# Kernel optimization log

Hardware: AMD Instinct MI355X
Metric: run time of the kernel (lower is better)

Reference implementation:

```python
import jax, jax.numpy as jnp
import numpy as np

N_HEADS = 16


def setup_inputs() -> dict:
    key = jax.random.key(0)
    ks = jax.random.split(key, 4)
    B, S, E = 4, 2048, 1024
    x = jax.random.normal(ks[0], (B, S, E), dtype=jnp.float32)
    w_attn = jax.random.normal(ks[1], (E, 3 * E), dtype=jnp.float32) * 0.02
    b_attn = jnp.zeros((3 * E,), dtype=jnp.float32)
    w_proj = jax.random.normal(ks[2], (E, E), dtype=jnp.float32) * 0.02
    b_proj = jnp.zeros((E,), dtype=jnp.float32)
    return {"x": x, "w_attn": w_attn, "b_attn": b_attn, "w_proj": w_proj, "b_proj": b_proj}


def reference(x, w_attn, b_attn, w_proj, b_proj):
    B, S, E = x.shape
    H = N_HEADS
    D = E // H
    # fused QKV projection (Conv1D: x @ W + b)
    qkv = x @ w_attn + b_attn                     # [B, S, 3E]
    q, k, v = jnp.split(qkv, 3, axis=-1)          # each [B, S, E]
    q = q.reshape(B, S, H, D).transpose(0, 2, 1, 3)  # [B, H, S, D]
    k = k.reshape(B, S, H, D).transpose(0, 2, 1, 3)
    v = v.reshape(B, S, H, D).transpose(0, 2, 1, 3)
    # scaled QK^T
    scores = jnp.einsum('bhqd,bhkd->bhqk', q, k) / jnp.sqrt(jnp.asarray(D, dtype=x.dtype))
    # causal mask via where with dtype-min fill (matches torch.where(c_m, w, finfo.min))
    causal = jnp.tril(jnp.ones((S, S), dtype=bool))  # [S, S]
    scores = jnp.where(causal[None, None, :, :], scores, jnp.finfo(scores.dtype).min)
    attn = jax.nn.softmax(scores, axis=-1)        # [B, H, S, S]
    o = jnp.einsum('bhqk,bhkd->bhqd', attn, v)    # [B, H, S, D]
    o = o.transpose(0, 2, 1, 3).reshape(B, S, E)  # merge heads
    return o @ w_proj + b_proj                    # output projection
```

## Files before the change

### kernel.cpp

```cpp
#include <hip/hip_runtime.h>
#include <stdint.h>


typedef __bf16 bf16;
typedef __bf16 bf16x4 __attribute__((ext_vector_type(4)));
typedef __bf16 bf16x8 __attribute__((ext_vector_type(8)));
typedef float  f32x4  __attribute__((ext_vector_type(4)));

#define DEV __device__ __forceinline__

DEV void async_copy16(bf16* lds, const bf16* g) {
  __builtin_amdgcn_global_load_lds(
      (__attribute__((address_space(1))) void*)(uintptr_t)g,
      (__attribute__((address_space(3))) void*)(uint32_t)(uintptr_t)lds,
      16, 0, 0);
}

__global__ __launch_bounds__(256) void cast_x_kernel(const float* __restrict__ in,
                                                     bf16* __restrict__ out, int n4) {
  int i = blockIdx.x * blockDim.x + threadIdx.x;
  int stride = gridDim.x * blockDim.x;
  for (; i < n4; i += stride) {
    float4 v = ((const float4*)in)[i];
    bf16x4 o = { (bf16)v.x, (bf16)v.y, (bf16)v.z, (bf16)v.w };
    *(bf16x4*)(out + (size_t)i * 4) = o;
  }
}

__global__ __launch_bounds__(256) void transpose_cast_kernel(const float* __restrict__ W,
                                                             bf16* __restrict__ Wt,
                                                             int Kd, int Nd) {
  __shared__ alignas(16) bf16 T[64 * 80];
  const int t = threadIdx.x;
  const int n0 = blockIdx.x * 64;
  const int k0 = blockIdx.y * 64;
#pragma unroll
  for (int i = 0; i < 4; ++i) {
    int idx = t + i * 256;
    int r  = idx >> 4;
    int c4 = (idx & 15) * 4;
    float4 v = *(const float4*)(W + (size_t)(k0 + r) * Nd + n0 + c4);
    bf16x4 o = { (bf16)v.x, (bf16)v.y, (bf16)v.z, (bf16)v.w };
    *(bf16x4*)(&T[r * 80 + c4]) = o;
  }
  __syncthreads();
#pragma unroll
  for (int i = 0; i < 2; ++i) {
    int idx = t + i * 256;
    int n = idx >> 3;
    int c = idx & 7;
    bf16x8 o;
#pragma unroll
    for (int j = 0; j < 8; ++j) o[j] = T[(c * 8 + j) * 80 + n];
    *(bf16x8*)(Wt + (size_t)(n0 + n) * Kd + k0 + c * 8) = o;
  }
}

__global__ __launch_bounds__(256) void vtrans_kernel(const bf16* __restrict__ qkv,
                                                     bf16* __restrict__ vt) {
  __shared__ alignas(16) bf16 T[64 * 80];
  const int t  = threadIdx.x;
  const int s0 = blockIdx.x * 64;
  const int bh = blockIdx.y;
  const int b = bh >> 4, h = bh & 15;
#pragma unroll
  for (int i = 0; i < 2; ++i) {
    int idx = t + i * 256;
    int s = idx >> 3, c = idx & 7;
    bf16x8 v = *(const bf16x8*)(qkv + (size_t)(b * 2048 + s0 + s) * 3072 + 2048 + h * 64 + c * 8);
    *(bf16x8*)(&T[s * 80 + c * 8]) = v;
  }
  __syncthreads();
#pragma unroll
  for (int i = 0; i < 2; ++i) {
    int idx = t + i * 256;
    int d = idx >> 3, c = idx & 7;
    bf16x8 o;
#pragma unroll
    for (int j = 0; j < 8; ++j) {
      int pos = c * 8 + j;
      int key = (pos & 32) | (((pos >> 2) & 1) << 4) | (((pos >> 3) & 3) << 2) | (pos & 3);
      o[j] = T[key * 80 + d];
    }
    *(bf16x8*)(vt + (size_t)(bh * 64 + d) * 2048 + s0 + c * 8) = o;
  }
}

template <typename OutT>
__global__ __launch_bounds__(512, 2) void gemm256_kernel(const bf16* __restrict__ A,
                                                         const bf16* __restrict__ Bt,
                                                         const float* __restrict__ bias,
                                                         OutT* __restrict__ C,
                                                         int M, int N, int K,
                                                         float qscale, int qcols,
                                                         int nbx) {
  __shared__ alignas(16) bf16 As[3][256 * 64];
  __shared__ alignas(16) bf16 Bs[3][128 * 64];

  const int tid  = threadIdx.x;
  const int lane = tid & 63;
  const int w    = tid >> 6;
  const int wm = w >> 1, wn = w & 1;
  const int l15 = lane & 15, l16 = lane >> 4;

  const int nwg = (int)gridDim.x;
  const int cpx = nwg >> 3;
  const int swz = ((int)blockIdx.x & 7) * cpx + ((int)blockIdx.x >> 3);
  const int m0 = (swz / nbx) * 256;
  const int n0 = (swz % nbx) * 128;

  const int srow = tid >> 3;
  const int sc   = tid & 7;
#define STAGE_HALF(buf, kt, H)                                                  \
  {                                                                             \
    const int k0_ = (kt) * 64;                                                  \
    _Pragma("unroll")                                                           \
    for (int j = 2 * (H); j < 2 * (H) + 2; ++j) {                               \
      int row = j * 64 + srow;                                                  \
      const bf16* src = A + (size_t)(m0 + row) * K + k0_ + 8 * (sc ^ (row & 7));\
      async_copy16(&As[buf][(j * 512 + w * 64) * 8], src);                      \
    }                                                                           \
    {                                                                           \
      int row = (H) * 64 + srow;                                                \
      const bf16* src = Bt + (size_t)(n0 + row) * K + k0_ + 8 * (sc ^ (row & 7));\
      async_copy16(&Bs[buf][((H) * 512 + w * 64) * 8], src);                    \
    }                                                                           \
  }

  f32x4 acc[4][4];
  f32x4 zf = {0.f, 0.f, 0.f, 0.f};
#pragma unroll
  for (int i = 0; i < 4; ++i)
#pragma unroll
    for (int j = 0; j < 4; ++j) acc[i][j] = zf;

  const int KT = K >> 6;
  STAGE_HALF(0, 0, 0) STAGE_HALF(0, 0, 1)
  STAGE_HALF(1, 1, 0) STAGE_HALF(1, 1, 1)

#define MFMA_HALF(buf, MLO)                                                     \
  {                                                                             \
    __builtin_amdgcn_s_setprio(1);                                              \
    _Pragma("unroll")                                                           \
    for (int m = (MLO); m < (MLO) + 2; ++m) {                                   \
      int ra = wm * 64 + m * 16 + l15;                                          \
      bf16x8 a0 = *(const bf16x8*)(&As[buf][ra * 64 + 8 * ((0 + l16) ^ (ra & 7))]); \
      bf16x8 a1 = *(const bf16x8*)(&As[buf][ra * 64 + 8 * ((4 + l16) ^ (ra & 7))]); \
      _Pragma("unroll")                                                         \
      for (int n = 0; n < 4; ++n)                                               \
        acc[m][n] = __builtin_amdgcn_mfma_f32_16x16x32_bf16(a0, bfr[n][0], acc[m][n], 0, 0, 0); \
      _Pragma("unroll")                                                         \
      for (int n = 0; n < 4; ++n)                                               \
        acc[m][n] = __builtin_amdgcn_mfma_f32_16x16x32_bf16(a1, bfr[n][1], acc[m][n], 0, 0, 0); \
    }                                                                           \
    __builtin_amdgcn_s_setprio(0);                                              \
  }

  int bufc = 0;
  int bufs = 2;
  for (int kt = 0; kt < KT - 1; ++kt) {
    asm volatile("s_waitcnt vmcnt(6)" ::: "memory");
    __builtin_amdgcn_s_barrier();
    asm volatile("" ::: "memory");
    const bool st = (kt + 2 < KT);
    if (st) STAGE_HALF(bufs, kt + 2, 0)
    bf16x8 bfr[4][2];
#pragma unroll
    for (int n = 0; n < 4; ++n) {
      int rb = wn * 64 + n * 16 + l15;
#pragma unroll
      for (int kk = 0; kk < 2; ++kk)
        bfr[n][kk] = *(const bf16x8*)(&Bs[bufc][rb * 64 + 8 * ((kk * 4 + l16) ^ (rb & 7))]);
    }
    MFMA_HALF(bufc, 0)
    asm volatile("" ::: "memory");
    __builtin_amdgcn_s_barrier();
    asm volatile("" ::: "memory");
    if (st) STAGE_HALF(bufs, kt + 2, 1)
    MFMA_HALF(bufc, 2)
    asm volatile("" ::: "memory");
    bufc = (bufc == 2) ? 0 : bufc + 1;
    bufs = (bufs == 2) ? 0 : bufs + 1;
  }
  asm volatile("s_waitcnt vmcnt(0)" ::: "memory");
  __builtin_amdgcn_s_barrier();
  asm volatile("" ::: "memory");
  {
    bf16x8 bfr[4][2];
#pragma unroll
    for (int n = 0; n < 4; ++n) {
      int rb = wn * 64 + n * 16 + l15;
#pragma unroll
      for (int kk = 0; kk < 2; ++kk)
        bfr[n][kk] = *(const bf16x8*)(&Bs[bufc][rb * 64 + 8 * ((kk * 4 + l16) ^ (rb & 7))]);
    }
    MFMA_HALF(bufc, 0)
    MFMA_HALF(bufc, 2)
  }

#pragma unroll
  for (int n = 0; n < 4; ++n) {
    int col = n0 + wn * 64 + n * 16 + l15;
    float bb = bias[col];
    float sc2 = (col < qcols) ? qscale : 1.0f;
#pragma unroll
    for (int m = 0; m < 4; ++m) {
#pragma unroll
      for (int reg = 0; reg < 4; ++reg) {
        int row = m0 + wm * 64 + m * 16 + l16 * 4 + reg;
        C[(size_t)row * N + col] = (OutT)((acc[m][n][reg] + bb) * sc2);
      }
    }
  }
#undef STAGE_HALF
#undef MFMA_HALF
}

__global__ __launch_bounds__(512, 4) void flash_kernel(const bf16* __restrict__ qkv,
                                                       const bf16* __restrict__ vt,
                                                       bf16* __restrict__ obuf) {
  constexpr int S = 2048, E3 = 3072;
  __shared__ alignas(16) bf16 Ks[2][64 * 64];
  __shared__ alignas(16) bf16 Vs[2][64 * 64];

  const int tid  = threadIdx.x;
  const int lane = tid & 63;
  const int w    = tid >> 6;
  const int bx = blockIdx.x;
  const int bh = blockIdx.y;
  const int b = bh >> 4, h = bh & 15;
  const int l15 = lane & 15, l16 = lane >> 4;

  const int sr  = w * 8 + (lane >> 3);
  const int scc = lane & 7;
  const bf16* kstage = qkv + (size_t)(b * S + sr) * E3 + 1024 + h * 64 + 8 * (scc ^ (sr & 7));
  const bf16* vstage = vt + (size_t)(bh * 64 + sr) * S + 8 * (scc ^ (sr & 7));

  const int xsw = l15 & 7;
  const uint32_t rdA = (uint32_t)(l15 * 128 + 16 * (l16 ^ xsw));
  const uint32_t rdB = (uint32_t)(l15 * 128 + 16 * ((4 + l16) ^ xsw));

#define KV_STAGE(buf, kv0_)                                        \
  {                                                                \
    async_copy16(Ks[buf] + w * 512, kstage + (size_t)(kv0_) * E3); \
    async_copy16(Vs[buf] + w * 512, vstage + (kv0_));              \
  }

  for (int half = 0; half < 2; ++half) {
    const int t = half ? (15 - bx) : bx;
    const int q0 = t * 128;
    const int wq0 = q0 + w * 16;
    const int nsteps = 2 * t + 2;

    KV_STAGE(0, 0)

    bf16x8 qf[2];
    {
      const bf16* qbase = qkv + (size_t)(b * S + wq0 + l15) * E3 + h * 64;
#pragma unroll
      for (int dk = 0; dk < 2; ++dk)
        qf[dk] = *(const bf16x8*)(qbase + (dk * 4 + l16) * 8);
    }

    float lstate = 0.f;
    f32x4 oacc[4];
    f32x4 zf = {0.f, 0.f, 0.f, 0.f};
#pragma unroll
    for (int i = 0; i < 4; ++i) oacc[i] = zf;

    __syncthreads();

#define FLASH_STEP(CUR, STEPIDX)                                                  \
    {                                                                             \
      const int kv0 = (STEPIDX) * 64;                                             \
      if ((STEPIDX) + 1 < nsteps) KV_STAGE((CUR) ^ 1, kv0 + 64)                   \
      if (kv0 <= wq0 + 15) {                     \
        f32x4 sv[4];                                                              \
        _Pragma("unroll")                                                         \
        for (int kf = 0; kf < 4; ++kf) sv[kf] = zf;                               \
        __builtin_amdgcn_s_setprio(1);                                            \
        _Pragma("unroll")                                                         \
        for (int kf = 0; kf < 4; ++kf) {                                          \
          bf16x8 k0 = *(const bf16x8*)((const char*)Ks[CUR] + rdA + kf * 2048);   \
          sv[kf] = __builtin_amdgcn_mfma_f32_16x16x32_bf16(k0, qf[0], sv[kf], 0, 0, 0); \
          bf16x8 k1 = *(const bf16x8*)((const char*)Ks[CUR] + rdB + kf * 2048);   \
          sv[kf] = __builtin_amdgcn_mfma_f32_16x16x32_bf16(k1, qf[1], sv[kf], 0, 0, 0); \
        }                                                                         \
        __builtin_amdgcn_s_setprio(0);                                            \
        if (kv0 + 63 > wq0) {     \
          const int qrow_ = wq0 + l15;                                            \
          _Pragma("unroll")                                                       \
          for (int kf = 0; kf < 4; ++kf)                                          \
            _Pragma("unroll")                                                     \
            for (int reg = 0; reg < 4; ++reg) {                                   \
              int key = kv0 + kf * 16 + l16 * 4 + reg;                            \
              if (key > qrow_) sv[kf][reg] = -1e30f;                              \
            }                                                                     \
        }                                                                         \
        float rsum = 0.f;                                                         \
        _Pragma("unroll")                                                         \
        for (int kf = 0; kf < 4; ++kf)                                            \
          _Pragma("unroll")                                                       \
          for (int reg = 0; reg < 4; ++reg) {                                     \
            float p = __builtin_amdgcn_exp2f(sv[kf][reg]);                        \
            sv[kf][reg] = p;                                                      \
            rsum += p;                                                            \
          }                                                                       \
        rsum += __shfl_xor(rsum, 16);                                             \
        rsum += __shfl_xor(rsum, 32);                                             \
        lstate += rsum;                                                           \
             \
        bf16x8 pb[2];                                                             \
        _Pragma("unroll")                                                         \
        for (int kc = 0; kc < 2; ++kc) {                                          \
          bf16x8 tq;                                                              \
          tq[0] = (bf16)sv[2 * kc][0];  tq[1] = (bf16)sv[2 * kc][1];              \
          tq[2] = (bf16)sv[2 * kc][2];  tq[3] = (bf16)sv[2 * kc][3];              \
          tq[4] = (bf16)sv[2 * kc + 1][0]; tq[5] = (bf16)sv[2 * kc + 1][1];       \
          tq[6] = (bf16)sv[2 * kc + 1][2]; tq[7] = (bf16)sv[2 * kc + 1][3];       \
          pb[kc] = tq;                                                            \
        }                                                                         \
        __builtin_amdgcn_s_setprio(1);                                            \
        _Pragma("unroll")                                                         \
        for (int nf = 0; nf < 4; ++nf) {                                          \
          bf16x8 vf0 = *(const bf16x8*)((const char*)Vs[CUR] + rdA + nf * 2048);  \
          oacc[nf] = __builtin_amdgcn_mfma_f32_16x16x32_bf16(vf0, pb[0], oacc[nf], 0, 0, 0); \
          bf16x8 vf1 = *(const bf16x8*)((const char*)Vs[CUR] + rdB + nf * 2048);  \
          oacc[nf] = __builtin_amdgcn_mfma_f32_16x16x32_bf16(vf1, pb[1], oacc[nf], 0, 0, 0); \
        }                                                                         \
        __builtin_amdgcn_s_setprio(0);                                            \
      }                                                                           \
      __syncthreads();          \
    }

    for (int step = 0; step < nsteps; step += 2) {
      FLASH_STEP(0, step)
      FLASH_STEP(1, step + 1)
    }
#undef FLASH_STEP

    float inv = 1.0f / lstate;
    int qrow = wq0 + l15;
#pragma unroll
    for (int nf = 0; nf < 4; ++nf) {
      bf16x4 o4 = { (bf16)(oacc[nf][0] * inv), (bf16)(oacc[nf][1] * inv),
                    (bf16)(oacc[nf][2] * inv), (bf16)(oacc[nf][3] * inv) };
      *(bf16x4*)(obuf + (size_t)(b * S + qrow) * 1024 + h * 64 + nf * 16 + l16 * 4) = o4;
    }
  }
#undef KV_STAGE
}

extern "C" void kernel_launch(void* const* d_in, const int* in_sizes, int n_in,
                              void* d_out, int out_size, void* d_ws, size_t ws_size,
                              hipStream_t stream) {
  (void)in_sizes; (void)n_in; (void)out_size; (void)ws_size;
  const float* x      = (const float*)d_in[0];
  const float* w_attn = (const float*)d_in[1];
  const float* b_attn = (const float*)d_in[2];
  const float* w_proj = (const float*)d_in[3];
  const float* b_proj = (const float*)d_in[4];
  float* out = (float*)d_out;

  char* ws = (char*)d_ws;
  bf16* xb  = (bf16*)(ws + 0);
  bf16* wat = (bf16*)(ws + 16777216);
  bf16* wpt = (bf16*)(ws + 23068672);
  bf16* qkv = (bf16*)(ws + 25165824);
  bf16* vt  = (bf16*)(ws + 75497472);
  bf16* ob  = (bf16*)(ws + 92274688);

  const float QSCALE = 0.18033688011112042f;

  cast_x_kernel<<<2048, 256, 0, stream>>>(x, xb, 8192 * 1024 / 4);
  transpose_cast_kernel<<<dim3(48, 16), 256, 0, stream>>>(w_attn, wat, 1024, 3072);
  transpose_cast_kernel<<<dim3(16, 16), 256, 0, stream>>>(w_proj, wpt, 1024, 1024);
  gemm256_kernel<bf16><<<768, 512, 0, stream>>>(xb, wat, b_attn, qkv,
                                                8192, 3072, 1024, QSCALE, 1024, 24);
  vtrans_kernel<<<dim3(32, 64), 256, 0, stream>>>(qkv, vt);
  flash_kernel<<<dim3(8, 64), 512, 0, stream>>>(qkv, vt, ob);
  gemm256_kernel<float><<<256, 512, 0, stream>>>(ob, wpt, b_proj, out,
                                                 8192, 1024, 1024, 1.0f, 0, 8);
}
```

Baseline: 163.6 us.

## Halve GEMM K-tile for higher occupancy and split flash blocks per query tile

The GEMM kernel's K-tile drops from 64 to 32, so LDS per block halves and launch bounds rise to 4 blocks per CU. The staging, swizzle and MFMA loop are restructured into one barrier per K step, with the tail folded into the main loop. The flash kernel no longer pairs a short and a long causal tile in one block. It launches one block per query tile, in reverse order, with higher launch bounds. This trades per-block load balancing and K-step amortization for more concurrent blocks, at some risk of register pressure and more barriers.

```diff
diff --git a/kernel.cpp b/kernel.cpp
--- a/kernel.cpp
+++ b/kernel.cpp
@@ -87,15 +87,15 @@
 }
 
 template <typename OutT>
-__global__ __launch_bounds__(512, 2) void gemm256_kernel(const bf16* __restrict__ A,
+__global__ __launch_bounds__(512, 4) void gemm256_kernel(const bf16* __restrict__ A,
                                                          const bf16* __restrict__ Bt,
                                                          const float* __restrict__ bias,
                                                          OutT* __restrict__ C,
                                                          int M, int N, int K,
                                                          float qscale, int qcols,
                                                          int nbx) {
-  __shared__ alignas(16) bf16 As[3][256 * 64];
-  __shared__ alignas(16) bf16 Bs[3][128 * 64];
+  __shared__ alignas(16) bf16 As[3][256 * 32];
+  __shared__ alignas(16) bf16 Bs[3][128 * 32];
 
   const int tid  = threadIdx.x;
   const int lane = tid & 63;
@@ -109,22 +109,19 @@
   const int m0 = (swz / nbx) * 256;
   const int n0 = (swz % nbx) * 128;
 
-  const int srow = tid >> 3;
-  const int sc   = tid & 7;
-#define STAGE_HALF(buf, kt, H)                                                  \
-  {                                                                             \
-    const int k0_ = (kt) * 64;                                                  \
-    _Pragma("unroll")                                                           \
-    for (int j = 2 * (H); j < 2 * (H) + 2; ++j) {                               \
-      int row = j * 64 + srow;                                                  \
-      const bf16* src = A + (size_t)(m0 + row) * K + k0_ + 8 * (sc ^ (row & 7));\
-      async_copy16(&As[buf][(j * 512 + w * 64) * 8], src);                      \
-    }                                                                           \
-    {                                                                           \
-      int row = (H) * 64 + srow;                                                \
-      const bf16* src = Bt + (size_t)(n0 + row) * K + k0_ + 8 * (sc ^ (row & 7));\
-      async_copy16(&Bs[buf][((H) * 512 + w * 64) * 8], src);                    \
-    }                                                                           \
+  const int c0  = w * 64 + lane;
+  const int rA0 = c0 >> 2, sA0 = c0 & 3;
+  const int rA1 = rA0 + 128;
+  const bf16* srcA0 = A  + (size_t)(m0 + rA0) * K + 8 * (sA0 ^ ((rA0 >> 1) & 3));
+  const bf16* srcA1 = A  + (size_t)(m0 + rA1) * K + 8 * (sA0 ^ ((rA1 >> 1) & 3));
+  const bf16* srcB  = Bt + (size_t)(n0 + rA0) * K + 8 * (sA0 ^ ((rA0 >> 1) & 3));
+
+#define STAGE_TILE(buf, kt)                                       \
+  {                                                               \
+    const int k0_ = (kt) * 32;                                    \
+    async_copy16(&As[buf][(w * 64) * 8],         srcA0 + k0_);    \
+    async_copy16(&As[buf][(512 + w * 64) * 8],   srcA1 + k0_);    \
+    async_copy16(&Bs[buf][(w * 64) * 8],         srcB  + k0_);    \
   }
 
   f32x4 acc[4][4];
@@ -134,68 +131,42 @@
 #pragma unroll
     for (int j = 0; j < 4; ++j) acc[i][j] = zf;
 
-  const int KT = K >> 6;
-  STAGE_HALF(0, 0, 0) STAGE_HALF(0, 0, 1)
-  STAGE_HALF(1, 1, 0) STAGE_HALF(1, 1, 1)
-
-#define MFMA_HALF(buf, MLO)                                                     \
-  {                                                                             \
-    __builtin_amdgcn_s_setprio(1);                                              \
-    _Pragma("unroll")                                                           \
-    for (int m = (MLO); m < (MLO) + 2; ++m) {                                   \
-      int ra = wm * 64 + m * 16 + l15;                                          \
-      bf16x8 a0 = *(const bf16x8*)(&As[buf][ra * 64 + 8 * ((0 + l16) ^ (ra & 7))]); \
-      bf16x8 a1 = *(const bf16x8*)(&As[buf][ra * 64 + 8 * ((4 + l16) ^ (ra & 7))]); \
-      _Pragma("unroll")                                                         \
-      for (int n = 0; n < 4; ++n)                                               \
-        acc[m][n] = __builtin_amdgcn_mfma_f32_16x16x32_bf16(a0, bfr[n][0], acc[m][n], 0, 0, 0); \
-      _Pragma("unroll")                                                         \
-      for (int n = 0; n < 4; ++n)                                               \
-        acc[m][n] = __builtin_amdgcn_mfma_f32_16x16x32_bf16(a1, bfr[n][1], acc[m][n], 0, 0, 0); \
-    }                                                                           \
-    __builtin_amdgcn_s_setprio(0);                                              \
-  }
+  const int KT = K >> 5;
+  STAGE_TILE(0, 0)
+  STAGE_TILE(1, 1)
+
+  const int soff = 8 * (l16 ^ ((l15 >> 1) & 3));
 
   int bufc = 0;
   int bufs = 2;
-  for (int kt = 0; kt < KT - 1; ++kt) {
-    asm volatile("s_waitcnt vmcnt(6)" ::: "memory");
+  for (int kt = 0; kt < KT; ++kt) {
+    if (kt < KT - 1) { asm volatile("s_waitcnt vmcnt(3)" ::: "memory"); }
+    else             { asm volatile("s_waitcnt vmcnt(0)" ::: "memory"); }
     __builtin_amdgcn_s_barrier();
     asm volatile("" ::: "memory");
-    const bool st = (kt + 2 < KT);
-    if (st) STAGE_HALF(bufs, kt + 2, 0)
-    bf16x8 bfr[4][2];
+    if (kt + 2 < KT) STAGE_TILE(bufs, kt + 2)
+
+    bf16x8 bfr[4], afr[4];
 #pragma unroll
     for (int n = 0; n < 4; ++n) {
       int rb = wn * 64 + n * 16 + l15;
-#pragma unroll
-      for (int kk = 0; kk < 2; ++kk)
-        bfr[n][kk] = *(const bf16x8*)(&Bs[bufc][rb * 64 + 8 * ((kk * 4 + l16) ^ (rb & 7))]);
-    }
-    MFMA_HALF(bufc, 0)
-    asm volatile("" ::: "memory");
-    __builtin_amdgcn_s_barrier();
-    asm volatile("" ::: "memory");
-    if (st) STAGE_HALF(bufs, kt + 2, 1)
-    MFMA_HALF(bufc, 2)
+      bfr[n] = *(const bf16x8*)(&Bs[bufc][rb * 32 + soff]);
+    }
+#pragma unroll
+    for (int m = 0; m < 4; ++m) {
+      int ra = wm * 64 + m * 16 + l15;
+      afr[m] = *(const bf16x8*)(&As[bufc][ra * 32 + soff]);
+    }
+    __builtin_amdgcn_s_setprio(1);
+#pragma unroll
+    for (int m = 0; m < 4; ++m)
+#pragma unroll
+      for (int n = 0; n < 4; ++n)
+        acc[m][n] = __builtin_amdgcn_mfma_f32_16x16x32_bf16(afr[m], bfr[n], acc[m][n], 0, 0, 0);
+    __builtin_amdgcn_s_setprio(0);
     asm volatile("" ::: "memory");
     bufc = (bufc == 2) ? 0 : bufc + 1;
     bufs = (bufs == 2) ? 0 : bufs + 1;
-  }
-  asm volatile("s_waitcnt vmcnt(0)" ::: "memory");
-  __builtin_amdgcn_s_barrier();
-  asm volatile("" ::: "memory");
-  {
-    bf16x8 bfr[4][2];
-#pragma unroll
-    for (int n = 0; n < 4; ++n) {
-      int rb = wn * 64 + n * 16 + l15;
-#pragma unroll
-      for (int kk = 0; kk < 2; ++kk)
-        bfr[n][kk] = *(const bf16x8*)(&Bs[bufc][rb * 64 + 8 * ((kk * 4 + l16) ^ (rb & 7))]);
-    }
-    MFMA_HALF(bufc, 0)
-    MFMA_HALF(bufc, 2)
   }
 
 #pragma unroll
@@ -212,11 +183,10 @@
       }
     }
   }
-#undef STAGE_HALF
-#undef MFMA_HALF
-}
-
-__global__ __launch_bounds__(512, 4) void flash_kernel(const bf16* __restrict__ qkv,
+#undef STAGE_TILE
+}
+
+__global__ __launch_bounds__(512, 6) void flash_kernel(const bf16* __restrict__ qkv,
                                                        const bf16* __restrict__ vt,
                                                        bf16* __restrict__ obuf) {
   constexpr int S = 2048, E3 = 3072;
@@ -226,7 +196,7 @@
   const int tid  = threadIdx.x;
   const int lane = tid & 63;
   const int w    = tid >> 6;
-  const int bx = blockIdx.x;
+  const int t  = 15 - (int)blockIdx.x;
   const int bh = blockIdx.y;
   const int b = bh >> 4, h = bh & 15;
   const int l15 = lane & 15, l16 = lane >> 4;
@@ -246,29 +216,27 @@
     async_copy16(Vs[buf] + w * 512, vstage + (kv0_));              \
   }
 
-  for (int half = 0; half < 2; ++half) {
-    const int t = half ? (15 - bx) : bx;
-    const int q0 = t * 128;
-    const int wq0 = q0 + w * 16;
-    const int nsteps = 2 * t + 2;
-
-    KV_STAGE(0, 0)
-
-    bf16x8 qf[2];
-    {
-      const bf16* qbase = qkv + (size_t)(b * S + wq0 + l15) * E3 + h * 64;
-#pragma unroll
-      for (int dk = 0; dk < 2; ++dk)
-        qf[dk] = *(const bf16x8*)(qbase + (dk * 4 + l16) * 8);
-    }
-
-    float lstate = 0.f;
-    f32x4 oacc[4];
-    f32x4 zf = {0.f, 0.f, 0.f, 0.f};
-#pragma unroll
-    for (int i = 0; i < 4; ++i) oacc[i] = zf;
-
-    __syncthreads();
+  const int q0 = t * 128;
+  const int wq0 = q0 + w * 16;
+  const int nsteps = 2 * t + 2;
+
+  KV_STAGE(0, 0)
+
+  bf16x8 qf[2];
+  {
+    const bf16* qbase = qkv + (size_t)(b * S + wq0 + l15) * E3 + h * 64;
+#pragma unroll
+    for (int dk = 0; dk < 2; ++dk)
+      qf[dk] = *(const bf16x8*)(qbase + (dk * 4 + l16) * 8);
+  }
+
+  float lstate = 0.f;
+  f32x4 oacc[4];
+  f32x4 zf = {0.f, 0.f, 0.f, 0.f};
+#pragma unroll
+  for (int i = 0; i < 4; ++i) oacc[i] = zf;
+
+  __syncthreads();
 
 #define FLASH_STEP(CUR, STEPIDX)                                                  \
     {                                                                             \
@@ -333,20 +301,19 @@
       __syncthreads();          \
     }
 
-    for (int step = 0; step < nsteps; step += 2) {
-      FLASH_STEP(0, step)
-      FLASH_STEP(1, step + 1)
-    }
+  for (int step = 0; step < nsteps; step += 2) {
+    FLASH_STEP(0, step)
+    FLASH_STEP(1, step + 1)
+  }
 #undef FLASH_STEP
 
-    float inv = 1.0f / lstate;
-    int qrow = wq0 + l15;
-#pragma unroll
-    for (int nf = 0; nf < 4; ++nf) {
-      bf16x4 o4 = { (bf16)(oacc[nf][0] * inv), (bf16)(oacc[nf][1] * inv),
-                    (bf16)(oacc[nf][2] * inv), (bf16)(oacc[nf][3] * inv) };
-      *(bf16x4*)(obuf + (size_t)(b * S + qrow) * 1024 + h * 64 + nf * 16 + l16 * 4) = o4;
-    }
+  float inv = 1.0f / lstate;
+  int qrow = wq0 + l15;
+#pragma unroll
+  for (int nf = 0; nf < 4; ++nf) {
+    bf16x4 o4 = { (bf16)(oacc[nf][0] * inv), (bf16)(oacc[nf][1] * inv),
+                  (bf16)(oacc[nf][2] * inv), (bf16)(oacc[nf][3] * inv) };
+    *(bf16x4*)(obuf + (size_t)(b * S + qrow) * 1024 + h * 64 + nf * 16 + l16 * 4) = o4;
   }
 #undef KV_STAGE
 }
@@ -378,7 +345,7 @@
   gemm256_kernel<bf16><<<768, 512, 0, stream>>>(xb, wat, b_attn, qkv,
                                                 8192, 3072, 1024, QSCALE, 1024, 24);
   vtrans_kernel<<<dim3(32, 64), 256, 0, stream>>>(qkv, vt);
-  flash_kernel<<<dim3(8, 64), 512, 0, stream>>>(qkv, vt, ob);
+  flash_kernel<<<dim3(16, 64), 512, 0, stream>>>(qkv, vt, ob);
   gemm256_kernel<float><<<256, 512, 0, stream>>>(ob, wpt, b_proj, out,
                                                  8192, 1024, 1024, 1.0f, 0, 8);
 }
```

After: 181.4 us. 10.9% more time.
